# Kernel tuning notes

Measured on AMD Instinct MI355X. Metric: run time of the kernel, lower is better.

The kernel has to match this reference:

```python
import jax, jax.numpy as jnp
import numpy as np

N, E, IN, H, OUT = 50000, 1600000, 128, 128, 16


def setup_inputs() -> dict:
    key = jax.random.key(0)
    ks = jax.random.split(key, 8)
    return {
        "x": jax.random.normal(ks[0], (N, IN), dtype=jnp.float32),
        "edge_index": jax.random.randint(ks[1], (2, E), 0, N, dtype=jnp.int64),
        "W1": jax.random.normal(ks[2], (IN, H), dtype=jnp.float32) * 0.05,
        "b1": jax.random.normal(ks[3], (H,), dtype=jnp.float32) * 0.05,
        "W2": jax.random.normal(ks[4], (H, H), dtype=jnp.float32) * 0.05,
        "b2": jax.random.normal(ks[5], (H,), dtype=jnp.float32) * 0.05,
        "Wc": jax.random.normal(ks[6], (H, OUT), dtype=jnp.float32) * 0.05,
        "bc": jax.random.normal(ks[7], (OUT,), dtype=jnp.float32) * 0.05,
    }


def _gcn_conv(x, src, dst, norm, W, b, n):
    # PyG GCNConv: h = x @ W; out[i] = sum_{(j->i)} norm_e * h[j]; out += b
    h = x @ W
    msg = h[src] * norm[:, None]          # [E+N, H] gather + scale
    out = jax.ops.segment_sum(msg, dst, num_segments=n)  # scatter-add
    return out + b


def reference(x, edge_index, W1, b1, W2, b2, Wc, bc):
    n = x.shape[0]
    loop = jnp.arange(n, dtype=edge_index.dtype)
    src = jnp.concatenate([edge_index[0], loop])  # add self-loops
    dst = jnp.concatenate([edge_index[1], loop])
    # symmetric normalization: deg over destinations (incl. self-loops)
    deg = jnp.zeros((n,), dtype=x.dtype).at[dst].add(1.0)
    d_inv_sqrt = jnp.where(deg > 0, jax.lax.rsqrt(deg), 0.0)
    norm = d_inv_sqrt[src] * d_inv_sqrt[dst]
    h = jax.nn.relu(_gcn_conv(x, src, dst, norm, W1, b1, n))
    # dropout p=0.5 is identity in eval mode
    h = jax.nn.relu(_gcn_conv(h, src, dst, norm, W2, b2, n))
    return h @ Wc + bc
```

## Files before the change

### kernel.cpp

```cpp
#include <hip/hip_runtime.h>
#include <hip/hip_bf16.h>


typedef unsigned int uint;

#define NPB 256
#define MAXBKT 256
#define CAP 12288

static __device__ __forceinline__ unsigned short f2bf(float f) {
    unsigned u = __float_as_uint(f);
    u += 0x7fffu + ((u >> 16) & 1u);
    return (unsigned short)(u >> 16);
}
static __device__ __forceinline__ uint pack2(float a, float b) {
    return (uint)f2bf(a) | ((uint)f2bf(b) << 16);
}
static __device__ __forceinline__ float lo2f(uint u) { return __uint_as_float(u << 16); }
static __device__ __forceinline__ float hi2f(uint u) { return __uint_as_float(u & 0xffff0000u); }

#define UNPACK8(dst, u)                                        \
    dst[0] = lo2f(u.x); dst[1] = hi2f(u.x);                    \
    dst[2] = lo2f(u.y); dst[3] = hi2f(u.y);                    \
    dst[4] = lo2f(u.z); dst[5] = hi2f(u.z);                    \
    dst[6] = lo2f(u.w); dst[7] = hi2f(u.w);


__global__ __launch_bounds__(256) void initcur(int* __restrict__ bcursor, int nbuckets) {
    int t = threadIdx.x;
    if (t < nbuckets) bcursor[t] = t * CAP;
}

__global__ __launch_bounds__(256) void bin_edges(const int* __restrict__ src,
                                                 const int* __restrict__ dst,
                                                 int* __restrict__ bcursor,
                                                 uint* __restrict__ pay,
                                                 int E, int nbuckets) {
    __shared__ int h[MAXBKT];
    __shared__ int base[MAXBKT];
    int tid = threadIdx.x;
    h[tid] = 0;
    __syncthreads();
    int chunk = (E + gridDim.x - 1) / gridDim.x;
    int i0 = blockIdx.x * chunk;
    int i1 = min(E, i0 + chunk);
    for (int i = i0 + tid; i < i1; i += 256) atomicAdd(&h[dst[i] >> 8], 1);
    __syncthreads();
    if (tid < nbuckets) base[tid] = h[tid] ? atomicAdd(&bcursor[tid], h[tid]) : 0;
    __syncthreads();
    h[tid] = 0;
    __syncthreads();
    for (int i = i0 + tid; i < i1; i += 256) {
        int d = dst[i];
        int b = d >> 8;
        int pos = base[b] + atomicAdd(&h[b], 1);
        pay[pos] = (uint)src[i] | ((uint)(d & 255) << 24);
    }
}

__global__ __launch_bounds__(256) void build_rows(const uint* __restrict__ pay,
                                                  const int* __restrict__ bcursor,
                                                  int* __restrict__ rowstart,
                                                  int* __restrict__ rowend,
                                                  float* __restrict__ dinv,
                                                  int* __restrict__ colidx, int n) {
    __shared__ int hist[NPB];
    __shared__ int sc[NPB];
    __shared__ int cur[NPB];
    int tid = threadIdx.x;
    int b = blockIdx.x;
    int node0 = b * NPB;
    int s = b * CAP, e = bcursor[b];

    hist[tid] = 0;
    __syncthreads();
    for (int i = s + tid; i < e; i += 256) atomicAdd(&hist[pay[i] >> 24], 1);
    __syncthreads();

    int v = hist[tid];
    sc[tid] = v;
    __syncthreads();
    for (int d = 1; d < 256; d <<= 1) {
        int x = (tid >= d) ? sc[tid - d] : 0;
        __syncthreads();
        sc[tid] += x;
        __syncthreads();
    }
    int excl = sc[tid] - v;
    cur[tid] = s + excl;
    int node = node0 + tid;
    if (node < n) {
        rowstart[node] = s + excl;
        rowend[node] = s + excl + v;
        dinv[node] = rsqrtf((float)(v + 1));
    }
    __syncthreads();

    for (int i = s + tid; i < e; i += 256) {
        uint p = pay[i];
        int pos = atomicAdd(&cur[p >> 24], 1);
        colidx[pos] = (int)(p & 0xffffffu);
    }
}

template <bool A_BF16>
__global__ __launch_bounds__(256) void gemm128(const void* __restrict__ Xv,
                                               const float* __restrict__ W,
                                               const float* __restrict__ dinv,
                                               uint* __restrict__ Yb, int n) {
    __shared__ float sW[32 * 128];
    const int tid = threadIdx.x;
    const int row0 = blockIdx.x * 64;
    const int ty = tid >> 4, tx = tid & 15;
    const int c0 = tx * 4;
    int r[4];
#pragma unroll
    for (int i = 0; i < 4; ++i) {
        int rr = row0 + ty * 4 + i;
        r[i] = rr < n ? rr : n - 1;
    }

    float acc[4][8];
#pragma unroll
    for (int i = 0; i < 4; ++i)
#pragma unroll
        for (int j = 0; j < 8; ++j) acc[i][j] = 0.f;

    for (int kc = 0; kc < 128; kc += 32) {
        __syncthreads();
        {
            const float4* W4 = (const float4*)(W + kc * 128);
            float4* s4 = (float4*)sW;
#pragma unroll
            for (int i = 0; i < 4; ++i) s4[tid + 256 * i] = W4[tid + 256 * i];
        }
        __syncthreads();

        for (int k4 = 0; k4 < 32; k4 += 4) {
            float a[4][4];
            if (A_BF16) {
                const uint2* X2 = (const uint2*)Xv;
#pragma unroll
                for (int i = 0; i < 4; ++i) {
                    uint2 u = X2[(size_t)r[i] * 32 + ((kc + k4) >> 2)];
                    a[i][0] = lo2f(u.x); a[i][1] = hi2f(u.x);
                    a[i][2] = lo2f(u.y); a[i][3] = hi2f(u.y);
                }
            } else {
                const float4* X4 = (const float4*)Xv;
#pragma unroll
                for (int i = 0; i < 4; ++i) {
                    float4 vv = X4[(size_t)r[i] * 32 + ((kc + k4) >> 2)];
                    a[i][0] = vv.x; a[i][1] = vv.y; a[i][2] = vv.z; a[i][3] = vv.w;
                }
            }
#pragma unroll
            for (int kk = 0; kk < 4; ++kk) {
                const int k = k4 + kk;
                float4 w0 = *(const float4*)&sW[k * 128 + c0];
                float4 w1 = *(const float4*)&sW[k * 128 + 64 + c0];
                float wv[8] = {w0.x, w0.y, w0.z, w0.w, w1.x, w1.y, w1.z, w1.w};
#pragma unroll
                for (int i = 0; i < 4; ++i) {
                    float av = a[i][kk];
#pragma unroll
                    for (int j = 0; j < 8; ++j) acc[i][j] = fmaf(av, wv[j], acc[i][j]);
                }
            }
        }
    }

#pragma unroll
    for (int i = 0; i < 4; ++i) {
        int rr = row0 + ty * 4 + i;
        if (rr < n) {
            float di = dinv[rr];
            uint2 o0 = {pack2(di * acc[i][0], di * acc[i][1]),
                        pack2(di * acc[i][2], di * acc[i][3])};
            uint2 o1 = {pack2(di * acc[i][4], di * acc[i][5]),
                        pack2(di * acc[i][6], di * acc[i][7])};
            *(uint2*)&Yb[(size_t)rr * 64 + (c0 >> 1)] = o0;
            *(uint2*)&Yb[(size_t)rr * 64 + 32 + (c0 >> 1)] = o1;
        }
    }
}

static __device__ __forceinline__ void gather_q(const uint4* __restrict__ H4,
                                                int s, int e, int nn, int sub,
                                                const int* __restrict__ colidx,
                                                float acc[8]) {
    uint4 su = H4[(size_t)nn * 16 + sub];
    UNPACK8(acc, su);

    int p = s;
    for (; p + 4 <= e; p += 4) {
        int c0 = colidx[p], c1 = colidx[p + 1], c2 = colidx[p + 2], c3 = colidx[p + 3];
        uint4 u0 = H4[(size_t)c0 * 16 + sub];
        uint4 u1 = H4[(size_t)c1 * 16 + sub];
        uint4 u2 = H4[(size_t)c2 * 16 + sub];
        uint4 u3 = H4[(size_t)c3 * 16 + sub];
        float a0[8], a1[8], a2[8], a3[8];
        UNPACK8(a0, u0);
        UNPACK8(a1, u1);
        UNPACK8(a2, u2);
        UNPACK8(a3, u3);
#pragma unroll
        for (int j = 0; j < 8; ++j) acc[j] += (a0[j] + a1[j]) + (a2[j] + a3[j]);
    }
    for (; p < e; ++p) {
        int c = colidx[p];
        uint4 u = H4[(size_t)c * 16 + sub];
        float a[8];
        UNPACK8(a, u);
#pragma unroll
        for (int j = 0; j < 8; ++j) acc[j] += a[j];
    }
}

__global__ __launch_bounds__(256) void agg_mid_q(const uint4* __restrict__ H4,
                                                 const int* __restrict__ rowstart,
                                                 const int* __restrict__ rowend,
                                                 const int* __restrict__ colidx,
                                                 const float* __restrict__ dinv,
                                                 const float* __restrict__ bias,
                                                 uint4* __restrict__ Ob, int n) {
    int tid = threadIdx.x;
    int sub = tid & 15;
    int node = blockIdx.x * 16 + (tid >> 4);
    int nn = node < n ? node : n - 1;
    int s = rowstart[nn], e = rowend[nn];
    float di = dinv[nn];

    float acc[8];
    gather_q(H4, s, e, nn, sub, colidx, acc);

    if (node < n) {
        float4 b0 = ((const float4*)bias)[sub * 2];
        float4 b1 = ((const float4*)bias)[sub * 2 + 1];
        float o0 = fmaxf(fmaf(acc[0], di, b0.x), 0.f);
        float o1 = fmaxf(fmaf(acc[1], di, b0.y), 0.f);
        float o2 = fmaxf(fmaf(acc[2], di, b0.z), 0.f);
        float o3 = fmaxf(fmaf(acc[3], di, b0.w), 0.f);
        float o4 = fmaxf(fmaf(acc[4], di, b1.x), 0.f);
        float o5 = fmaxf(fmaf(acc[5], di, b1.y), 0.f);
        float o6 = fmaxf(fmaf(acc[6], di, b1.z), 0.f);
        float o7 = fmaxf(fmaf(acc[7], di, b1.w), 0.f);
        uint4 ov;
        ov.x = pack2(o0, o1); ov.y = pack2(o2, o3);
        ov.z = pack2(o4, o5); ov.w = pack2(o6, o7);
        Ob[(size_t)node * 16 + sub] = ov;
    }
}

__global__ __launch_bounds__(256) void agg_out_q(const uint4* __restrict__ H4,
                                                 const int* __restrict__ rowstart,
                                                 const int* __restrict__ rowend,
                                                 const int* __restrict__ colidx,
                                                 const float* __restrict__ dinv,
                                                 const float* __restrict__ bias,
                                                 const float* __restrict__ Wc,
                                                 const float* __restrict__ bc,
                                                 float* __restrict__ out, int n) {
    __shared__ float sA[16][129];
    int tid = threadIdx.x;
    int sub = tid & 15;
    int nl = tid >> 4;
    int node = blockIdx.x * 16 + nl;
    int nn = node < n ? node : n - 1;
    int s = rowstart[nn], e = rowend[nn];
    float di = dinv[nn];

    float acc[8];
    gather_q(H4, s, e, nn, sub, colidx, acc);

    {
        float4 b0 = ((const float4*)bias)[sub * 2];
        float4 b1 = ((const float4*)bias)[sub * 2 + 1];
        float f[8];
        f[0] = fmaxf(fmaf(acc[0], di, b0.x), 0.f);
        f[1] = fmaxf(fmaf(acc[1], di, b0.y), 0.f);
        f[2] = fmaxf(fmaf(acc[2], di, b0.z), 0.f);
        f[3] = fmaxf(fmaf(acc[3], di, b0.w), 0.f);
        f[4] = fmaxf(fmaf(acc[4], di, b1.x), 0.f);
        f[5] = fmaxf(fmaf(acc[5], di, b1.y), 0.f);
        f[6] = fmaxf(fmaf(acc[6], di, b1.z), 0.f);
        f[7] = fmaxf(fmaf(acc[7], di, b1.w), 0.f);
#pragma unroll
        for (int j = 0; j < 8; ++j) sA[nl][sub * 8 + j] = f[j];
    }
    __syncthreads();

    int col = tid & 15;
    float p0 = 0.f, p1 = 0.f;
#pragma unroll 4
    for (int k = 0; k < 128; k += 2) {
        p0 = fmaf(sA[nl][k], Wc[k * 16 + col], p0);
        p1 = fmaf(sA[nl][k + 1], Wc[(k + 1) * 16 + col], p1);
    }
    if (node < n) out[(size_t)node * 16 + col] = p0 + p1 + bc[col];
}


extern "C" void kernel_launch(void* const* d_in, const int* in_sizes, int n_in,
                              void* d_out, int out_size, void* d_ws, size_t ws_size,
                              hipStream_t stream) {
    const float* x  = (const float*)d_in[0];
    const int*   ei = (const int*)d_in[1];
    const float* W1 = (const float*)d_in[2];
    const float* b1 = (const float*)d_in[3];
    const float* W2 = (const float*)d_in[4];
    const float* b2 = (const float*)d_in[5];
    const float* Wc = (const float*)d_in[6];
    const float* bc = (const float*)d_in[7];
    float* out = (float*)d_out;

    const int n = in_sizes[0] / 128;
    const int E = in_sizes[1] / 2;
    const int* src = ei;
    const int* dst = ei + E;
    const int nbuckets = (n + NPB - 1) / NPB;

    char* p = (char*)d_ws;
    auto alloc = [&](size_t bytes) {
        char* q = p;
        p += (bytes + 255) & ~(size_t)255;
        return q;
    };
    int*   bcursor  = (int*)alloc(MAXBKT * 4);
    int*   rowstart = (int*)alloc((size_t)n * 4);
    int*   rowend   = (int*)alloc((size_t)n * 4);
    float* dinv     = (float*)alloc((size_t)n * 4);
    uint*  pay      = (uint*)alloc((size_t)nbuckets * CAP * 4);
    int*   colidx   = (int*)alloc((size_t)nbuckets * CAP * 4);
    uint*  bufA     = (uint*)alloc((size_t)n * 64 * 4);
    uint*  bufB     = (uint*)alloc((size_t)n * 64 * 4);
    if ((size_t)(p - (char*)d_ws) > ws_size) return;

    initcur<<<1, 256, 0, stream>>>(bcursor, nbuckets);
    bin_edges<<<256, 256, 0, stream>>>(src, dst, bcursor, pay, E, nbuckets);
    build_rows<<<nbuckets, 256, 0, stream>>>(pay, bcursor, rowstart, rowend, dinv, colidx, n);

    const int gemmb = (n + 63) / 64;
    const int aggb = (n + 15) / 16;
    gemm128<false><<<gemmb, 256, 0, stream>>>(x, W1, dinv, bufA, n);
    agg_mid_q<<<aggb, 256, 0, stream>>>((const uint4*)bufA, rowstart, rowend, colidx,
                                        dinv, b1, (uint4*)bufB, n);
    gemm128<true><<<gemmb, 256, 0, stream>>>(bufB, W2, dinv, bufA, n);
    agg_out_q<<<aggb, 256, 0, stream>>>((const uint4*)bufA, rowstart, rowend, colidx,
                                        dinv, b2, Wc, bc, out, n);
}
```

Baseline: 301.8 us.

## Use bf16 MFMA for dense GEMMs and widen gather unroll to eight

Replaces the FP32 SIMT 128x128 GEMMs with bf16 MFMA 16x16x32 kernels. A small prep kernel transposes and converts W1/W2 to bf16, and each wave computes a 16-row tile, staging output through LDS for coalesced stores. The edge gather loop is unrolled from 4 to 8 loads in flight, with the tail padded using the self row and corrected by subtraction. Rounding x and W to bf16 adds precision loss, and the tail correction can add small rounding error.

```diff
diff --git a/kernel.cpp b/kernel.cpp
--- a/kernel.cpp
+++ b/kernel.cpp
@@ -3,15 +3,18 @@
 
 
 typedef unsigned int uint;
+typedef unsigned short ushort;
+typedef __attribute__((ext_vector_type(8))) short bf16x8;
+typedef __attribute__((ext_vector_type(4))) float f32x4;
 
 #define NPB 256
 #define MAXBKT 256
 #define CAP 12288
 
-static __device__ __forceinline__ unsigned short f2bf(float f) {
+static __device__ __forceinline__ ushort f2bf(float f) {
     unsigned u = __float_as_uint(f);
     u += 0x7fffu + ((u >> 16) & 1u);
-    return (unsigned short)(u >> 16);
+    return (ushort)(u >> 16);
 }
 static __device__ __forceinline__ uint pack2(float a, float b) {
     return (uint)f2bf(a) | ((uint)f2bf(b) << 16);
@@ -103,84 +106,77 @@
     }
 }
 
+__global__ __launch_bounds__(256) void prep_wt(const float* __restrict__ W1,
+                                               const float* __restrict__ W2,
+                                               ushort* __restrict__ Wt1,
+                                               ushort* __restrict__ Wt2) {
+    int idx = blockIdx.x * 256 + threadIdx.x;
+    int k = idx >> 7, nn = idx & 127;
+    Wt1[nn * 128 + k] = f2bf(W1[idx]);
+    Wt2[nn * 128 + k] = f2bf(W2[idx]);
+}
+
 template <bool A_BF16>
-__global__ __launch_bounds__(256) void gemm128(const void* __restrict__ Xv,
-                                               const float* __restrict__ W,
-                                               const float* __restrict__ dinv,
-                                               uint* __restrict__ Yb, int n) {
-    __shared__ float sW[32 * 128];
-    const int tid = threadIdx.x;
-    const int row0 = blockIdx.x * 64;
-    const int ty = tid >> 4, tx = tid & 15;
-    const int c0 = tx * 4;
-    int r[4];
+__global__ __launch_bounds__(256) void gemm_mfma(const void* __restrict__ Xv,
+                                                 const ushort* __restrict__ Wt,
+                                                 const float* __restrict__ dinv,
+                                                 uint* __restrict__ Yb, int n) {
+    __shared__ __align__(16) ushort sOut[4][16][136];
+    const int wave = threadIdx.x >> 6;
+    const int lane = threadIdx.x & 63;
+    const int quad = lane >> 4, l16 = lane & 15;
+    const int m0 = blockIdx.x * 64 + wave * 16;
+
+    f32x4 acc[8];
+#pragma unroll
+    for (int t = 0; t < 8; ++t) acc[t] = (f32x4){0.f, 0.f, 0.f, 0.f};
+
+    int arow = m0 + l16;
+    arow = arow < n ? arow : n - 1;
+
+#pragma unroll
+    for (int ks = 0; ks < 4; ++ks) {
+        bf16x8 a;
+        if (A_BF16) {
+            const ushort* X = (const ushort*)Xv;
+            a = *(const bf16x8*)&X[(size_t)arow * 128 + ks * 32 + quad * 8];
+        } else {
+            const float* X = (const float*)Xv;
+            const float* px = &X[(size_t)arow * 128 + ks * 32 + quad * 8];
+            float4 x0 = *(const float4*)px;
+            float4 x1 = *(const float4*)(px + 4);
+            ushort av[8] = {f2bf(x0.x), f2bf(x0.y), f2bf(x0.z), f2bf(x0.w),
+                            f2bf(x1.x), f2bf(x1.y), f2bf(x1.z), f2bf(x1.w)};
+            a = *(const bf16x8*)av;
+        }
+#pragma unroll
+        for (int nt = 0; nt < 8; ++nt) {
+            bf16x8 b = *(const bf16x8*)&Wt[(size_t)(nt * 16 + l16) * 128 + ks * 32 + quad * 8];
+            acc[nt] = __builtin_amdgcn_mfma_f32_16x16x32_bf16(a, b, acc[nt], 0, 0, 0);
+        }
+    }
+
+    float dv[4];
+#pragma unroll
+    for (int r = 0; r < 4; ++r) {
+        int rr = m0 + quad * 4 + r;
+        dv[r] = dinv[rr < n ? rr : n - 1];
+    }
+#pragma unroll
+    for (int nt = 0; nt < 8; ++nt)
+#pragma unroll
+        for (int r = 0; r < 4; ++r)
+            sOut[wave][quad * 4 + r][nt * 16 + l16] = f2bf(acc[nt][r] * dv[r]);
+    __syncthreads();
+
 #pragma unroll
     for (int i = 0; i < 4; ++i) {
-        int rr = row0 + ty * 4 + i;
-        r[i] = rr < n ? rr : n - 1;
-    }
-
-    float acc[4][8];
-#pragma unroll
-    for (int i = 0; i < 4; ++i)
-#pragma unroll
-        for (int j = 0; j < 8; ++j) acc[i][j] = 0.f;
-
-    for (int kc = 0; kc < 128; kc += 32) {
-        __syncthreads();
-        {
-            const float4* W4 = (const float4*)(W + kc * 128);
-            float4* s4 = (float4*)sW;
-#pragma unroll
-            for (int i = 0; i < 4; ++i) s4[tid + 256 * i] = W4[tid + 256 * i];
-        }
-        __syncthreads();
-
-        for (int k4 = 0; k4 < 32; k4 += 4) {
-            float a[4][4];
-            if (A_BF16) {
-                const uint2* X2 = (const uint2*)Xv;
-#pragma unroll
-                for (int i = 0; i < 4; ++i) {
-                    uint2 u = X2[(size_t)r[i] * 32 + ((kc + k4) >> 2)];
-                    a[i][0] = lo2f(u.x); a[i][1] = hi2f(u.x);
-                    a[i][2] = lo2f(u.y); a[i][3] = hi2f(u.y);
-                }
-            } else {
-                const float4* X4 = (const float4*)Xv;
-#pragma unroll
-                for (int i = 0; i < 4; ++i) {
-                    float4 vv = X4[(size_t)r[i] * 32 + ((kc + k4) >> 2)];
-                    a[i][0] = vv.x; a[i][1] = vv.y; a[i][2] = vv.z; a[i][3] = vv.w;
-                }
-            }
-#pragma unroll
-            for (int kk = 0; kk < 4; ++kk) {
-                const int k = k4 + kk;
-                float4 w0 = *(const float4*)&sW[k * 128 + c0];
-                float4 w1 = *(const float4*)&sW[k * 128 + 64 + c0];
-                float wv[8] = {w0.x, w0.y, w0.z, w0.w, w1.x, w1.y, w1.z, w1.w};
-#pragma unroll
-                for (int i = 0; i < 4; ++i) {
-                    float av = a[i][kk];
-#pragma unroll
-                    for (int j = 0; j < 8; ++j) acc[i][j] = fmaf(av, wv[j], acc[i][j]);
-                }
-            }
-        }
-    }
-
-#pragma unroll
-    for (int i = 0; i < 4; ++i) {
-        int rr = row0 + ty * 4 + i;
+        int linear = i * 64 + lane;
+        int row = linear >> 4, chunk = linear & 15;
+        int rr = m0 + row;
         if (rr < n) {
-            float di = dinv[rr];
-            uint2 o0 = {pack2(di * acc[i][0], di * acc[i][1]),
-                        pack2(di * acc[i][2], di * acc[i][3])};
-            uint2 o1 = {pack2(di * acc[i][4], di * acc[i][5]),
-                        pack2(di * acc[i][6], di * acc[i][7])};
-            *(uint2*)&Yb[(size_t)rr * 64 + (c0 >> 1)] = o0;
-            *(uint2*)&Yb[(size_t)rr * 64 + 32 + (c0 >> 1)] = o1;
+            uint4 v = *(const uint4*)&sOut[wave][row][chunk * 8];
+            *(uint4*)&Yb[(size_t)rr * 64 + chunk * 4] = v;
         }
     }
 }
@@ -190,30 +186,44 @@
                                                 const int* __restrict__ colidx,
                                                 float acc[8]) {
     uint4 su = H4[(size_t)nn * 16 + sub];
-    UNPACK8(acc, su);
+    float t[8];
+    UNPACK8(t, su);
+#pragma unroll
+    for (int j = 0; j < 8; ++j) acc[j] = t[j];
 
     int p = s;
-    for (; p + 4 <= e; p += 4) {
-        int c0 = colidx[p], c1 = colidx[p + 1], c2 = colidx[p + 2], c3 = colidx[p + 3];
-        uint4 u0 = H4[(size_t)c0 * 16 + sub];
-        uint4 u1 = H4[(size_t)c1 * 16 + sub];
-        uint4 u2 = H4[(size_t)c2 * 16 + sub];
-        uint4 u3 = H4[(size_t)c3 * 16 + sub];
-        float a0[8], a1[8], a2[8], a3[8];
-        UNPACK8(a0, u0);
-        UNPACK8(a1, u1);
-        UNPACK8(a2, u2);
-        UNPACK8(a3, u3);
-#pragma unroll
-        for (int j = 0; j < 8; ++j) acc[j] += (a0[j] + a1[j]) + (a2[j] + a3[j]);
-    }
-    for (; p < e; ++p) {
-        int c = colidx[p];
-        uint4 u = H4[(size_t)c * 16 + sub];
-        float a[8];
-        UNPACK8(a, u);
-#pragma unroll
-        for (int j = 0; j < 8; ++j) acc[j] += a[j];
+    for (; p + 8 <= e; p += 8) {
+        int c[8];
+#pragma unroll
+        for (int i = 0; i < 8; ++i) c[i] = colidx[p + i];
+        uint4 u[8];
+#pragma unroll
+        for (int i = 0; i < 8; ++i) u[i] = H4[(size_t)c[i] * 16 + sub];
+#pragma unroll
+        for (int i = 0; i < 8; ++i) {
+            float a[8];
+            UNPACK8(a, u[i]);
+#pragma unroll
+            for (int j = 0; j < 8; ++j) acc[j] += a[j];
+        }
+    }
+    if (p < e) {
+        int c[8];
+#pragma unroll
+        for (int i = 0; i < 8; ++i) c[i] = (p + i < e) ? colidx[p + i] : nn;
+        uint4 u[8];
+#pragma unroll
+        for (int i = 0; i < 8; ++i) u[i] = H4[(size_t)c[i] * 16 + sub];
+#pragma unroll
+        for (int i = 0; i < 8; ++i) {
+            float a[8];
+            UNPACK8(a, u[i]);
+#pragma unroll
+            for (int j = 0; j < 8; ++j) acc[j] += a[j];
+        }
+        float pad = (float)(p + 8 - e);
+#pragma unroll
+        for (int j = 0; j < 8; ++j) acc[j] -= pad * t[j];
     }
 }
 
@@ -326,26 +336,29 @@
         p += (bytes + 255) & ~(size_t)255;
         return q;
     };
-    int*   bcursor  = (int*)alloc(MAXBKT * 4);
-    int*   rowstart = (int*)alloc((size_t)n * 4);
-    int*   rowend   = (int*)alloc((size_t)n * 4);
-    float* dinv     = (float*)alloc((size_t)n * 4);
-    uint*  pay      = (uint*)alloc((size_t)nbuckets * CAP * 4);
-    int*   colidx   = (int*)alloc((size_t)nbuckets * CAP * 4);
-    uint*  bufA     = (uint*)alloc((size_t)n * 64 * 4);
-    uint*  bufB     = (uint*)alloc((size_t)n * 64 * 4);
+    int*    bcursor  = (int*)alloc(MAXBKT * 4);
+    int*    rowstart = (int*)alloc((size_t)n * 4);
+    int*    rowend   = (int*)alloc((size_t)n * 4);
+    float*  dinv     = (float*)alloc((size_t)n * 4);
+    ushort* Wt1      = (ushort*)alloc(128 * 128 * 2);
+    ushort* Wt2      = (ushort*)alloc(128 * 128 * 2);
+    uint*   pay      = (uint*)alloc((size_t)nbuckets * CAP * 4);
+    int*    colidx   = (int*)alloc((size_t)nbuckets * CAP * 4);
+    uint*   bufA     = (uint*)alloc((size_t)n * 64 * 4);
+    uint*   bufB     = (uint*)alloc((size_t)n * 64 * 4);
     if ((size_t)(p - (char*)d_ws) > ws_size) return;
 
     initcur<<<1, 256, 0, stream>>>(bcursor, nbuckets);
     bin_edges<<<256, 256, 0, stream>>>(src, dst, bcursor, pay, E, nbuckets);
     build_rows<<<nbuckets, 256, 0, stream>>>(pay, bcursor, rowstart, rowend, dinv, colidx, n);
+    prep_wt<<<64, 256, 0, stream>>>(W1, W2, Wt1, Wt2);
 
     const int gemmb = (n + 63) / 64;
     const int aggb = (n + 15) / 16;
-    gemm128<false><<<gemmb, 256, 0, stream>>>(x, W1, dinv, bufA, n);
+    gemm_mfma<false><<<gemmb, 256, 0, stream>>>(x, Wt1, dinv, bufA, n);
     agg_mid_q<<<aggb, 256, 0, stream>>>((const uint4*)bufA, rowstart, rowend, colidx,
                                         dinv, b1, (uint4*)bufB, n);
-    gemm128<true><<<gemmb, 256, 0, stream>>>(bufB, W2, dinv, bufA, n);
+    gemm_mfma<true><<<gemmb, 256, 0, stream>>>(bufB, Wt2, dinv, bufA, n);
     agg_out_q<<<aggb, 256, 0, stream>>>((const uint4*)bufA, rowstart, rowend, colidx,
                                         dinv, b2, Wc, bc, out, n);
 }
```

After: 284.8 us. -5.6%, faster.
